# Kernel optimization log

Measured on AMD Instinct MI355X. Metric: run time of the kernel, lower is better.

The kernel has to match this reference:

```python
import jax, jax.numpy as jnp
import numpy as np

BN_EPS = 1e-5


def setup_inputs() -> dict:
    key = jax.random.key(0)
    ks = jax.random.split(key, 8)
    B, N, D = 16, 16384, 64
    NP, NS = 1024, 32
    inp = {
        "xyz": jax.random.normal(ks[0], (B, 3, N), dtype=jnp.float32),
        "points": jax.random.normal(ks[1], (B, D, N), dtype=jnp.float32),
        "fps_init": jax.random.randint(ks[2], (B,), 0, N, dtype=jnp.int32),
        "group_idx": jax.random.randint(ks[3], (B, NP, NS), 0, N, dtype=jnp.int32),
    }
    chans = [67, 64, 128, 128]
    for i in range(3):
        cin, cout = chans[i], chans[i + 1]
        wk = jax.random.fold_in(ks[4], i)
        inp[f"W{i}"] = jax.random.normal(wk, (cout, cin), dtype=jnp.float32) * (1.0 / np.sqrt(cin))
        inp[f"b{i}"] = jnp.zeros((cout,), dtype=jnp.float32)
        inp[f"g{i}"] = jnp.ones((cout,), dtype=jnp.float32)
        inp[f"be{i}"] = jnp.zeros((cout,), dtype=jnp.float32)
    return inp


def _fps(x, init_far, npoint):
    # x: [B,N,3]; iterative furthest point sampling, npoint sequential steps
    B, N, _ = x.shape

    def step(carry, _):
        dist, far = carry
        c = jnp.take_along_axis(x, far[:, None, None], axis=1)  # [B,1,3]
        d = jnp.sum((x - c) ** 2, axis=-1)                       # [B,N]
        dist = jnp.minimum(dist, d)
        return (dist, jnp.argmax(dist, axis=-1).astype(far.dtype)), far

    init = (jnp.full((B, N), 1e10, dtype=x.dtype), init_far)
    _, cents = jax.lax.scan(step, init, None, length=npoint)
    return cents.T  # [B, npoint]


def _conv_bn_relu(h, W, b, g, be):
    # h: [B, np, ns, Cin]; 1x1 conv == channel matmul; BN (training stats) over (B,np,ns)
    y = jnp.einsum('bskc,oc->bsko', h, W) + b
    m = y.mean(axis=(0, 1, 2))
    v = y.var(axis=(0, 1, 2))
    y = (y - m) * jax.lax.rsqrt(v + BN_EPS) * g + be
    return jax.nn.relu(y)


def reference(xyz, points, fps_init, group_idx,
              W0, b0, g0, be0, W1, b1, g1, be1, W2, b2, g2, be2):
    x = jnp.transpose(xyz, (0, 2, 1))     # [B,N,3]
    p = jnp.transpose(points, (0, 2, 1))  # [B,N,D]
    B, N, _ = x.shape
    NP, NS = group_idx.shape[1], group_idx.shape[2]

    cents = _fps(x, fps_init, NP)                                   # [B,NP]
    new_xyz = jnp.take_along_axis(x, cents[:, :, None], axis=1)     # [B,NP,3]

    flat = group_idx.reshape(B, NP * NS)
    gx = jnp.take_along_axis(x, flat[:, :, None], axis=1).reshape(B, NP, NS, 3)
    gp = jnp.take_along_axis(p, flat[:, :, None], axis=1).reshape(B, NP, NS, -1)
    h = jnp.concatenate([gx, gp], axis=-1)  # [B,NP,NS,67]

    h = _conv_bn_relu(h, W0, b0, g0, be0)
    h = _conv_bn_relu(h, W1, b1, g1, be1)
    h = _conv_bn_relu(h, W2, b2, g2, be2)
    new_points = h.max(axis=2)              # max over nsample -> [B,NP,Cout]

    return jnp.transpose(new_xyz, (0, 2, 1)), jnp.transpose(new_points, (0, 2, 1))
```

## Files before the change

kernel.cpp:

```cpp
#include <hip/hip_runtime.h>

typedef short bf16x8 __attribute__((ext_vector_type(8)));
typedef float f32x4 __attribute__((ext_vector_type(4)));
typedef float f32x2 __attribute__((ext_vector_type(2)));
typedef unsigned short u16;
typedef unsigned int u32;
typedef unsigned long long u64;

#define NPTS 16384
#define NPOINT 1024
#define STOT 524288
#define NCB 240
#define NW  960

__device__ __forceinline__ u16 f2bf(float f){
  u32 u = __builtin_bit_cast(u32, f);
  u += 0x7fffu + ((u >> 16) & 1u);
  return (u16)(u >> 16);
}
__device__ __forceinline__ float bf2f(u16 u){
  u32 x = ((u32)u) << 16;
  return __builtin_bit_cast(float, x);
}

template<int CTRL>
__device__ __forceinline__ float dpp_maxf(float v){
  int x = __builtin_amdgcn_update_dpp(0, __builtin_bit_cast(int, v), CTRL, 0xf, 0xf, true);
  return fmaxf(v, __builtin_bit_cast(float, x));
}
template<int CTRL>
__device__ __forceinline__ u64 dpp_max(u64 key){
  u32 lo = (u32)key, hi = (u32)(key >> 32);
  u32 lo1 = (u32)__builtin_amdgcn_update_dpp(0, (int)lo, CTRL, 0xf, 0xf, true);
  u32 hi1 = (u32)__builtin_amdgcn_update_dpp(0, (int)hi, CTRL, 0xf, 0xf, true);
  u64 k1 = ((u64)hi1 << 32) | (u64)lo1;
  return (k1 > key) ? k1 : key;
}
__device__ __forceinline__ u64 packkey(float d, int idx){
  return ((u64)__builtin_bit_cast(u32, d) << 32) | (u64)(u32)(~(u32)idx);
}

__device__ __forceinline__ void arrive(u32* c){
  __hip_atomic_fetch_add(c, 1u, __ATOMIC_RELEASE, __HIP_MEMORY_SCOPE_AGENT);
}
__device__ __forceinline__ void waitc(u32* c, u32 tgt){
  while (__hip_atomic_load(c, __ATOMIC_ACQUIRE, __HIP_MEMORY_SCOPE_AGENT) < tgt)
    __builtin_amdgcn_s_sleep(16);
}

struct FpsS  { u32 rec[2][16][48]; uint2 kk[2][16]; float cbuf[NPOINT][3]; };
struct ConvS { float lsum[128]; float lsqr[128]; float av[128]; float dv[128]; };
union SMemU  { FpsS fps; ConvS conv; };

__device__ __forceinline__ bf16x8 load_bn_relu(const u16* __restrict__ row, int ko,
                                               const float* __restrict__ av,
                                               const float* __restrict__ dv){
  uint4 r = *(const uint4*)(row + ko);
  u32 w[4] = {r.x, r.y, r.z, r.w};
  bf16x8 out;
#pragma unroll
  for (int jj = 0; jj < 8; jj++){
    u16 us = (u16)(w[jj >> 1] >> ((jj & 1) * 16));
    float h = fmaxf(fmaf(av[ko + jj], bf2f(us), dv[ko + jj]), 0.f);
    out[jj] = (short)f2bf(h);
  }
  return out;
}

__global__ void zero_kernel(u32* __restrict__ ctrs){
  if (threadIdx.x < 64) ctrs[threadIdx.x] = 0;
}

__global__ __launch_bounds__(1024, 4) void mega_kernel(
    const float* __restrict__ xyz, const float* __restrict__ points,
    const int* __restrict__ finit, const int* __restrict__ gidx,
    const float* __restrict__ W0, const float* __restrict__ g0v, const float* __restrict__ be0,
    const float* __restrict__ W1, const float* __restrict__ g1v, const float* __restrict__ be1,
    const float* __restrict__ W2, const float* __restrict__ g2v, const float* __restrict__ be2,
    float* __restrict__ out0, float* __restrict__ out1,
    u16* __restrict__ XP, u16* __restrict__ y0, u16* __restrict__ y1,
    float* __restrict__ maxb, float* __restrict__ minb,
    float* __restrict__ statsF,
    u16* __restrict__ W0bf, u16* __restrict__ W1bf, u16* __restrict__ W2bf,
    u32* __restrict__ ctrs){
  __shared__ SMemU sm;
  const int t = threadIdx.x;
  const int wave = t >> 6, lane = t & 63;

  if (blockIdx.x < 16){
    const int b = blockIdx.x;
    const float* xb = xyz + (size_t)b * 3 * NPTS;
    f32x2 px[8], py[8], pz[8], dist[8];
#pragma unroll
    for (int j = 0; j < 8; j++){
      f32x2 x, y, z;
#pragma unroll
      for (int h = 0; h < 2; h++){
        int n = ((2*j + h) << 10) + t;
        x[h] = xb[n];
        y[h] = xb[NPTS + n];
        z[h] = xb[2*NPTS + n];
      }
      px[j] = x; py[j] = y; pz[j] = z;
      f32x2 big = {1e10f, 1e10f};
      dist[j] = big;
    }
    const int far0 = finit[b];
    float ccx = xb[far0], ccy = xb[NPTS + far0], ccz = xb[2*NPTS + far0];

    for (int it = 0; it < NPOINT; it++){
      const int p = it & 1;
      if (t == 0){
        sm.fps.cbuf[it][0] = ccx;
        sm.fps.cbuf[it][1] = ccy;
        sm.fps.cbuf[it][2] = ccz;
      }
      float bv = -1.f; int bk = 0;
      {
#pragma clang fp contract(off)
        f32x2 cx2 = {ccx, ccx}, cy2 = {ccy, ccy}, cz2 = {ccz, ccz};
#pragma unroll
        for (int j = 0; j < 8; j++){
          f32x2 dx = px[j] - cx2;
          f32x2 dy = py[j] - cy2;
          f32x2 dz = pz[j] - cz2;
          f32x2 dd = dx*dx + dy*dy + dz*dz;
          f32x2 dm = __builtin_elementwise_min(dist[j], dd);
          dist[j] = dm;
          bool g0 = dm.x > bv;
          bv = g0 ? dm.x : bv;  bk = g0 ? (2*j)   : bk;
          bool g1 = dm.y > bv;
          bv = g1 ? dm.y : bv;  bk = g1 ? (2*j+1) : bk;
        }
      }
      float m = bv;
      m = dpp_maxf<0xB1>(m);
      m = dpp_maxf<0x4E>(m);
      m = dpp_maxf<0x141>(m);
      m = dpp_maxf<0x140>(m);
      m = dpp_maxf<0x142>(m);
      m = dpp_maxf<0x143>(m);
      float ms = __builtin_bit_cast(float, __builtin_amdgcn_readlane(__builtin_bit_cast(int, m), 63));
      u64 mk = __ballot(bv == ms);
      int wl;
      if (__popcll(mk) == 1){
        wl = (int)__builtin_ctzll(mk);
      } else {
        u64 key = packkey(bv, (bk << 10) + t);
        key = dpp_max<0xB1>(key); key = dpp_max<0x4E>(key);
        key = dpp_max<0x141>(key); key = dpp_max<0x140>(key);
        key = dpp_max<0x142>(key); key = dpp_max<0x143>(key);
        u32 lo = (u32)__builtin_amdgcn_readlane((int)(u32)key, 63);
        wl = (int)((~lo) & 63u);
      }
      if (lane == wl){
        u32* r = &sm.fps.rec[p][wave][0];
#pragma unroll
        for (int j = 0; j < 8; j++){
          *(f32x2*)(r + 2*j)      = px[j];
          *(f32x2*)(r + 16 + 2*j) = py[j];
          *(f32x2*)(r + 32 + 2*j) = pz[j];
        }
        u64 key = packkey(bv, (bk << 10) + t);
        sm.fps.kk[p][wave] = make_uint2((u32)key, (u32)(key >> 32));
      }
      __syncthreads();
      uint2 wkk = sm.fps.kk[p][lane & 15];
      u64 gk = ((u64)wkk.y << 32) | (u64)wkk.x;
      gk = dpp_max<0xB1>(gk); gk = dpp_max<0x4E>(gk);
      gk = dpp_max<0x141>(gk); gk = dpp_max<0x140>(gk);
      u32 n = ~(u32)gk;
      int w    = (int)((n >> 6) & 15u);
      int kwin = (int)(n >> 10);
      const u32* rr = &sm.fps.rec[p][w][0];
      ccx = *(const float*)(rr + kwin);
      ccy = *(const float*)(rr + 16 + kwin);
      ccz = *(const float*)(rr + 32 + kwin);
    }
    for (int i = t; i < 3 * NPOINT; i += 1024){
      int cc = i >> 10, itt = i & 1023;
      out0[((size_t)b*3 + cc)*NPOINT + itt] = sm.fps.cbuf[itt][cc];
    }
    return;
  }

  const int cb = blockIdx.x - 16;
  const int lw = wave & 3, g = wave >> 2;
  const int Wk = cb*4 + g;
  const int lrow = lane & 15, lq = lane >> 4;
  float* bsum0 = statsF;          float* bsqr0 = statsF + 8192;
  float* bsum1 = statsF + 16384;  float* bsqr1 = statsF + 24576;
  float* bsum2 = statsF + 32768;  float* bsqr2 = statsF + 40960;
  float* a0 = statsF + 49152;       float* d0 = a0 + 128;
  float* a1 = statsF + 49152 + 256; float* d1 = a1 + 128;
  float* a2 = statsF + 49152 + 512; float* d2 = a2 + 128;

  for (u32 idx = (u32)cb*1024u + t; idx < 16u*16384u; idx += (u32)NCB*1024u){
    u32 b = idx >> 14, n = idx & 16383u;
    const float* xb = xyz + (size_t)b*3*NPTS + n;
    const float* pb = points + (size_t)b*64*NPTS + n;
    u16* dst = XP + ((size_t)b*NPTS + n)*96;
#pragma unroll
    for (int half = 0; half < 2; half++){
      u32 w[24];
#pragma unroll
      for (int q = 0; q < 24; q++){
        int c0 = half*48 + 2*q, c1 = c0 + 1;
        float f0 = (c0 < 3) ? xb[(size_t)c0*NPTS] : (c0 < 67) ? pb[(size_t)(c0-3)*NPTS] : 0.f;
        float f1 = (c1 < 3) ? xb[(size_t)c1*NPTS] : (c1 < 67) ? pb[(size_t)(c1-3)*NPTS] : 0.f;
        w[q] = (u32)f2bf(f0) | ((u32)f2bf(f1) << 16);
      }
#pragma unroll
      for (int q = 0; q < 6; q++){
        uint4 v; v.x = w[4*q]; v.y = w[4*q+1]; v.z = w[4*q+2]; v.w = w[4*q+3];
        *(uint4*)(dst + half*48 + q*8) = v;
      }
    }
  }
  if (cb == 0){
    for (int i = t; i < 64*96; i += 1024){
      int nn = i / 96, kk = i % 96;
      W0bf[i] = (kk < 67) ? f2bf(W0[nn*67 + kk]) : (u16)0;
    }
    for (int i = t; i < 128*64; i += 1024) W1bf[i] = f2bf(W1[i]);
    for (int i = t; i < 128*128; i += 1024) W2bf[i] = f2bf(W2[i]);
  }
  if (cb == 1){
    for (int i = t; i < 49152; i += 1024) statsF[i] = 0.f;
  }
  __threadfence();
  __syncthreads();
  if (t == 0){ arrive(&ctrs[0]); waitc(&ctrs[0], NCB); }
  __syncthreads();

  if (t < 128){ sm.conv.lsum[t] = 0.f; sm.conv.lsqr[t] = 0.f; }
  __syncthreads();
  for (int j2 = Wk; j2 < 4096; j2 += NW){
    const int b = j2 >> 8;
    const size_t srow = (size_t)j2 * 128;
    const int gbase = b*32768 + (j2 & 255)*128;
    const int m0 = lw*32 + lrow, m1 = m0 + 16;
    const int p0 = gidx[gbase + m0];
    const int p1 = gidx[gbase + m1];
    const bf16x8* ar0 = (const bf16x8*)(XP + ((size_t)b*NPTS + p0)*96);
    const bf16x8* ar1 = (const bf16x8*)(XP + ((size_t)b*NPTS + p1)*96);
    f32x4 acc[2][4];
#pragma unroll
    for (int mt = 0; mt < 2; mt++)
#pragma unroll
      for (int nt = 0; nt < 4; nt++){ f32x4 z = {0.f,0.f,0.f,0.f}; acc[mt][nt] = z; }
#pragma unroll
    for (int ks = 0; ks < 3; ks++){
      bf16x8 af0 = ar0[ks*4 + lq];
      bf16x8 af1 = ar1[ks*4 + lq];
#pragma unroll
      for (int nt = 0; nt < 4; nt++){
        bf16x8 bb = *(const bf16x8*)(W0bf + (nt*16 + lrow)*96 + ks*32 + lq*8);
        acc[0][nt] = __builtin_amdgcn_mfma_f32_16x16x32_bf16(af0, bb, acc[0][nt], 0, 0, 0);
        acc[1][nt] = __builtin_amdgcn_mfma_f32_16x16x32_bf16(af1, bb, acc[1][nt], 0, 0, 0);
      }
    }
#pragma unroll
    for (int nt = 0; nt < 4; nt++){
      float s = 0.f, s2 = 0.f;
#pragma unroll
      for (int mt = 0; mt < 2; mt++){
#pragma unroll
        for (int i = 0; i < 4; i++){
          float u = acc[mt][nt][i];
          s += u; s2 = fmaf(u, u, s2);
          int m = lw*32 + mt*16 + lq*4 + i;
          y0[(srow + m)*64 + nt*16 + lrow] = f2bf(u);
        }
      }
      s  += __shfl_xor(s, 16, 64);  s  += __shfl_xor(s, 32, 64);
      s2 += __shfl_xor(s2, 16, 64); s2 += __shfl_xor(s2, 32, 64);
      if (lane < 16){ atomicAdd(&sm.conv.lsum[nt*16 + lane], s); atomicAdd(&sm.conv.lsqr[nt*16 + lane], s2); }
    }
  }
  __syncthreads();
  if (t < 64){
    atomicAdd(&bsum0[(cb & 63)*128 + t], sm.conv.lsum[t]);
    atomicAdd(&bsqr0[(cb & 63)*128 + t], sm.conv.lsqr[t]);
  }
  __threadfence();
  __syncthreads();
  if (t == 0) arrive(&ctrs[1]);
  if (cb == 0){
    if (t == 0) waitc(&ctrs[1], NCB);
    __syncthreads();
    if (t < 64){
      float s = 0.f, s2 = 0.f;
      for (int k = 0; k < 64; k++){ s += bsum0[k*128 + t]; s2 += bsqr0[k*128 + t]; }
      const float inv = 1.f / (float)STOT;
      float m = s * inv, v = s2 * inv - m*m;
      float aa = g0v[t] / sqrtf(v + 1e-5f);
      a0[t] = aa; d0[t] = be0[t] - m*aa;
    }
    __threadfence();
    __syncthreads();
    if (t == 0) arrive(&ctrs[2]);
  }
  if (t == 0) waitc(&ctrs[2], 1);
  __syncthreads();

  if (t < 128){ sm.conv.lsum[t] = 0.f; sm.conv.lsqr[t] = 0.f; }
  if (t < 64){ sm.conv.av[t] = a0[t]; sm.conv.dv[t] = d0[t]; }
  __syncthreads();
  for (int j2 = Wk; j2 < 4096; j2 += NW){
    const size_t srow = (size_t)j2 * 128;
    const int m0 = lw*32 + lrow, m1 = m0 + 16;
    const u16* row0 = y0 + (srow + m0)*64;
    const u16* row1 = y0 + (srow + m1)*64;
    f32x4 acc[2][8];
#pragma unroll
    for (int mt = 0; mt < 2; mt++)
#pragma unroll
      for (int nt = 0; nt < 8; nt++){ f32x4 z = {0.f,0.f,0.f,0.f}; acc[mt][nt] = z; }
#pragma unroll
    for (int ks = 0; ks < 2; ks++){
      const int ko = ks*32 + lq*8;
      bf16x8 af0 = load_bn_relu(row0, ko, sm.conv.av, sm.conv.dv);
      bf16x8 af1 = load_bn_relu(row1, ko, sm.conv.av, sm.conv.dv);
#pragma unroll
      for (int nt = 0; nt < 8; nt++){
        bf16x8 bb = *(const bf16x8*)(W1bf + (nt*16 + lrow)*64 + ko);
        acc[0][nt] = __builtin_amdgcn_mfma_f32_16x16x32_bf16(af0, bb, acc[0][nt], 0, 0, 0);
        acc[1][nt] = __builtin_amdgcn_mfma_f32_16x16x32_bf16(af1, bb, acc[1][nt], 0, 0, 0);
      }
    }
#pragma unroll
    for (int nt = 0; nt < 8; nt++){
      float s = 0.f, s2 = 0.f;
#pragma unroll
      for (int mt = 0; mt < 2; mt++){
#pragma unroll
        for (int i = 0; i < 4; i++){
          float u = acc[mt][nt][i];
          s += u; s2 = fmaf(u, u, s2);
          int m = lw*32 + mt*16 + lq*4 + i;
          y1[(srow + m)*128 + nt*16 + lrow] = f2bf(u);
        }
      }
      s  += __shfl_xor(s, 16, 64);  s  += __shfl_xor(s, 32, 64);
      s2 += __shfl_xor(s2, 16, 64); s2 += __shfl_xor(s2, 32, 64);
      if (lane < 16){ atomicAdd(&sm.conv.lsum[nt*16 + lane], s); atomicAdd(&sm.conv.lsqr[nt*16 + lane], s2); }
    }
  }
  __syncthreads();
  if (t < 128){
    atomicAdd(&bsum1[(cb & 63)*128 + t], sm.conv.lsum[t]);
    atomicAdd(&bsqr1[(cb & 63)*128 + t], sm.conv.lsqr[t]);
  }
  __threadfence();
  __syncthreads();
  if (t == 0) arrive(&ctrs[3]);
  if (cb == 0){
    if (t == 0) waitc(&ctrs[3], NCB);
    __syncthreads();
    if (t < 128){
      float s = 0.f, s2 = 0.f;
      for (int k = 0; k < 64; k++){ s += bsum1[k*128 + t]; s2 += bsqr1[k*128 + t]; }
      const float inv = 1.f / (float)STOT;
      float m = s * inv, v = s2 * inv - m*m;
      float aa = g1v[t] / sqrtf(v + 1e-5f);
      a1[t] = aa; d1[t] = be1[t] - m*aa;
    }
    __threadfence();
    __syncthreads();
    if (t == 0) arrive(&ctrs[4]);
  }
  if (t == 0) waitc(&ctrs[4], 1);
  __syncthreads();

  if (t < 128){ sm.conv.lsum[t] = 0.f; sm.conv.lsqr[t] = 0.f;
                sm.conv.av[t] = a1[t]; sm.conv.dv[t] = d1[t]; }
  __syncthreads();
  for (int j2 = Wk; j2 < 4096; j2 += NW){
    const size_t srow = (size_t)j2 * 128;
    const int m0 = lw*32 + lrow, m1 = m0 + 16;
    const u16* row0 = y1 + (srow + m0)*128;
    const u16* row1 = y1 + (srow + m1)*128;
    f32x4 acc[2][8];
#pragma unroll
    for (int mt = 0; mt < 2; mt++)
#pragma unroll
      for (int nt = 0; nt < 8; nt++){ f32x4 z = {0.f,0.f,0.f,0.f}; acc[mt][nt] = z; }
#pragma unroll
    for (int ks = 0; ks < 4; ks++){
      const int ko = ks*32 + lq*8;
      bf16x8 af0 = load_bn_relu(row0, ko, sm.conv.av, sm.conv.dv);
      bf16x8 af1 = load_bn_relu(row1, ko, sm.conv.av, sm.conv.dv);
#pragma unroll
      for (int nt = 0; nt < 8; nt++){
        bf16x8 bb = *(const bf16x8*)(W2bf + (nt*16 + lrow)*128 + ko);
        acc[0][nt] = __builtin_amdgcn_mfma_f32_16x16x32_bf16(af0, bb, acc[0][nt], 0, 0, 0);
        acc[1][nt] = __builtin_amdgcn_mfma_f32_16x16x32_bf16(af1, bb, acc[1][nt], 0, 0, 0);
      }
    }
#pragma unroll
    for (int nt = 0; nt < 8; nt++){
      float s = 0.f, s2 = 0.f, mx = -3.4e38f, mn = 3.4e38f;
#pragma unroll
      for (int mt = 0; mt < 2; mt++){
#pragma unroll
        for (int i = 0; i < 4; i++){
          float u = acc[mt][nt][i];
          s += u; s2 = fmaf(u, u, s2);
          mx = fmaxf(mx, u); mn = fminf(mn, u);
        }
      }
      s  += __shfl_xor(s, 16, 64);  s  += __shfl_xor(s, 32, 64);
      s2 += __shfl_xor(s2, 16, 64); s2 += __shfl_xor(s2, 32, 64);
      mx = fmaxf(mx, __shfl_xor(mx, 16, 64)); mx = fmaxf(mx, __shfl_xor(mx, 32, 64));
      mn = fminf(mn, __shfl_xor(mn, 16, 64)); mn = fminf(mn, __shfl_xor(mn, 32, 64));
      if (lane < 16){
        size_t gi = ((size_t)j2*4 + lw)*128 + nt*16 + lane;
        maxb[gi] = mx; minb[gi] = mn;
        atomicAdd(&sm.conv.lsum[nt*16 + lane], s); atomicAdd(&sm.conv.lsqr[nt*16 + lane], s2);
      }
    }
  }
  __syncthreads();
  if (t < 128){
    atomicAdd(&bsum2[(cb & 63)*128 + t], sm.conv.lsum[t]);
    atomicAdd(&bsqr2[(cb & 63)*128 + t], sm.conv.lsqr[t]);
  }
  __threadfence();
  __syncthreads();
  if (t == 0) arrive(&ctrs[5]);
  if (cb == 0){
    if (t == 0) waitc(&ctrs[5], NCB);
    __syncthreads();
    if (t < 128){
      float s = 0.f, s2 = 0.f;
      for (int k = 0; k < 64; k++){ s += bsum2[k*128 + t]; s2 += bsqr2[k*128 + t]; }
      const float inv = 1.f / (float)STOT;
      float m = s * inv, v = s2 * inv - m*m;
      float aa = g2v[t] / sqrtf(v + 1e-5f);
      a2[t] = aa; d2[t] = be2[t] - m*aa;
    }
    __threadfence();
    __syncthreads();
    if (t == 0) arrive(&ctrs[6]);
  }
  if (t == 0) waitc(&ctrs[6], 1);
  __syncthreads();

  for (u32 e = (u32)cb*1024u + t; e < 16u*1024u*128u; e += (u32)NCB*1024u){
    u32 np = e & 1023u;
    u32 c  = (e >> 10) & 127u;
    u32 b  = e >> 17;
    size_t gi = ((size_t)b*1024 + np)*128 + c;
    float a = a2[c];
    float v = (a >= 0.f) ? maxb[gi] : minb[gi];
    out1[((size_t)b*128 + c)*1024 + np] = fmaxf(fmaf(a, v, d2[c]), 0.f);
  }
}

extern "C" void kernel_launch(void* const* d_in, const int* in_sizes, int n_in,
                              void* d_out, int out_size, void* d_ws, size_t ws_size,
                              hipStream_t stream) {
  const float* xyz    = (const float*)d_in[0];
  const float* points = (const float*)d_in[1];
  const int*   finit  = (const int*)d_in[2];
  const int*   gidx   = (const int*)d_in[3];
  const float* W0  = (const float*)d_in[4];
  const float* g0v = (const float*)d_in[6];
  const float* be0 = (const float*)d_in[7];
  const float* W1  = (const float*)d_in[8];
  const float* g1v = (const float*)d_in[10];
  const float* be1 = (const float*)d_in[11];
  const float* W2  = (const float*)d_in[12];
  const float* g2v = (const float*)d_in[14];
  const float* be2 = (const float*)d_in[15];

  float* out0 = (float*)d_out;
  float* out1 = out0 + 16*3*NPOINT;

  char* ws = (char*)d_ws;
  u16* y1 = (u16*)ws;
  u16* XP = (u16*)ws;
  u16* y0 = (u16*)(ws + 134217728);
  float* maxb = (float*)(ws + 134217728);
  float* minb = (float*)(ws + 134217728 + 8388608);
  float* statsF = (float*)(ws + 201326592);
  u16* W0bf = (u16*)(ws + 201326592 + 49920*4);
  u16* W1bf = W0bf + 64*96;
  u16* W2bf = W1bf + 128*64;
  u32* ctrs = (u32*)(ws + 205782016);

  zero_kernel<<<1, 64, 0, stream>>>(ctrs);
  mega_kernel<<<256, 1024, 0, stream>>>(
      xyz, points, finit, gidx,
      W0, g0v, be0, W1, g1v, be1, W2, g2v, be2,
      out0, out1, XP, y0, y1, maxb, minb, statsF,
      W0bf, W1bf, W2bf, ctrs);
}
```

Baseline: 1.972 ms.

## Restructure FPS to 512 threads with y/z coordinates in LDS and readlane broadcast

```diff
diff --git a/kernel.cpp b/kernel.cpp
--- a/kernel.cpp
+++ b/kernel.cpp
@@ -2,7 +2,6 @@
 
 typedef short bf16x8 __attribute__((ext_vector_type(8)));
 typedef float f32x4 __attribute__((ext_vector_type(4)));
-typedef float f32x2 __attribute__((ext_vector_type(2)));
 typedef unsigned short u16;
 typedef unsigned int u32;
 typedef unsigned long long u64;
@@ -12,6 +11,9 @@
 #define STOT 524288
 #define NCB 240
 #define NW  960
+#define FTHREADS 512
+#define FWAVES 8
+#define KPT 32
 
 __device__ __forceinline__ u16 f2bf(float f){
   u32 u = __builtin_bit_cast(u32, f);
@@ -48,7 +50,13 @@
     __builtin_amdgcn_s_sleep(16);
 }
 
-struct FpsS  { u32 rec[2][16][48]; uint2 kk[2][16]; float cbuf[NPOINT][3]; };
+struct FpsS  {
+  float ylds[KPT][FTHREADS];
+  float zlds[KPT][FTHREADS];
+  float cbuf[NPOINT][3];
+  float kxA[2][FWAVES], kyA[2][FWAVES], kzA[2][FWAVES];
+  uint2 kkA[2][FWAVES];
+};
 struct ConvS { float lsum[128]; float lsqr[128]; float av[128]; float dv[128]; };
 union SMemU  { FpsS fps; ConvS conv; };
 
@@ -88,25 +96,21 @@
   const int wave = t >> 6, lane = t & 63;
 
   if (blockIdx.x < 16){
+    if (t >= FTHREADS) return;
     const int b = blockIdx.x;
     const float* xb = xyz + (size_t)b * 3 * NPTS;
-    f32x2 px[8], py[8], pz[8], dist[8];
-#pragma unroll
-    for (int j = 0; j < 8; j++){
-      f32x2 x, y, z;
-#pragma unroll
-      for (int h = 0; h < 2; h++){
-        int n = ((2*j + h) << 10) + t;
-        x[h] = xb[n];
-        y[h] = xb[NPTS + n];
-        z[h] = xb[2*NPTS + n];
-      }
-      px[j] = x; py[j] = y; pz[j] = z;
-      f32x2 big = {1e10f, 1e10f};
-      dist[j] = big;
+    float px[KPT], dist[KPT];
+#pragma unroll
+    for (int k = 0; k < KPT; k++){
+      int n = (k << 9) + t;
+      px[k] = xb[n];
+      sm.fps.ylds[k][t] = xb[NPTS + n];
+      sm.fps.zlds[k][t] = xb[2*NPTS + n];
+      dist[k] = 1e10f;
     }
     const int far0 = finit[b];
     float ccx = xb[far0], ccy = xb[NPTS + far0], ccz = xb[2*NPTS + far0];
+    __syncthreads();
 
     for (int it = 0; it < NPOINT; it++){
       const int p = it & 1;
@@ -118,19 +122,16 @@
       float bv = -1.f; int bk = 0;
       {
 #pragma clang fp contract(off)
-        f32x2 cx2 = {ccx, ccx}, cy2 = {ccy, ccy}, cz2 = {ccz, ccz};
-#pragma unroll
-        for (int j = 0; j < 8; j++){
-          f32x2 dx = px[j] - cx2;
-          f32x2 dy = py[j] - cy2;
-          f32x2 dz = pz[j] - cz2;
-          f32x2 dd = dx*dx + dy*dy + dz*dz;
-          f32x2 dm = __builtin_elementwise_min(dist[j], dd);
-          dist[j] = dm;
-          bool g0 = dm.x > bv;
-          bv = g0 ? dm.x : bv;  bk = g0 ? (2*j)   : bk;
-          bool g1 = dm.y > bv;
-          bv = g1 ? dm.y : bv;  bk = g1 ? (2*j+1) : bk;
+#pragma unroll
+        for (int k = 0; k < KPT; k++){
+          float dx = px[k] - ccx;
+          float dy = sm.fps.ylds[k][t] - ccy;
+          float dz = sm.fps.zlds[k][t] - ccz;
+          float dd = dx*dx + dy*dy + dz*dz;
+          float dm = fminf(dist[k], dd);
+          dist[k] = dm;
+          bool g = dm > bv;
+          bv = g ? dm : bv;  bk = g ? k : bk;
         }
       }
       float m = bv;
@@ -146,7 +147,7 @@
       if (__popcll(mk) == 1){
         wl = (int)__builtin_ctzll(mk);
       } else {
-        u64 key = packkey(bv, (bk << 10) + t);
+        u64 key = packkey(bv, (bk << 9) + t);
         key = dpp_max<0xB1>(key); key = dpp_max<0x4E>(key);
         key = dpp_max<0x141>(key); key = dpp_max<0x140>(key);
         key = dpp_max<0x142>(key); key = dpp_max<0x143>(key);
@@ -154,30 +155,31 @@
         wl = (int)((~lo) & 63u);
       }
       if (lane == wl){
-        u32* r = &sm.fps.rec[p][wave][0];
-#pragma unroll
-        for (int j = 0; j < 8; j++){
-          *(f32x2*)(r + 2*j)      = px[j];
-          *(f32x2*)(r + 16 + 2*j) = py[j];
-          *(f32x2*)(r + 32 + 2*j) = pz[j];
-        }
-        u64 key = packkey(bv, (bk << 10) + t);
-        sm.fps.kk[p][wave] = make_uint2((u32)key, (u32)(key >> 32));
+        int kk2 = bk;
+        float sx = px[0];
+#pragma unroll
+        for (int k2 = 1; k2 < KPT; k2++){ bool e = (kk2 == k2); sx = e ? px[k2] : sx; }
+        sm.fps.kxA[p][wave] = sx;
+        sm.fps.kyA[p][wave] = sm.fps.ylds[kk2][t];
+        sm.fps.kzA[p][wave] = sm.fps.zlds[kk2][t];
+        u64 key = packkey(bv, (bk << 9) + t);
+        sm.fps.kkA[p][wave] = make_uint2((u32)key, (u32)(key >> 32));
       }
       __syncthreads();
-      uint2 wkk = sm.fps.kk[p][lane & 15];
+      const int sl = lane & 7;
+      uint2 wkk = sm.fps.kkA[p][sl];
+      u32 fx = __builtin_bit_cast(u32, sm.fps.kxA[p][sl]);
+      u32 fy = __builtin_bit_cast(u32, sm.fps.kyA[p][sl]);
+      u32 fz = __builtin_bit_cast(u32, sm.fps.kzA[p][sl]);
       u64 gk = ((u64)wkk.y << 32) | (u64)wkk.x;
-      gk = dpp_max<0xB1>(gk); gk = dpp_max<0x4E>(gk);
-      gk = dpp_max<0x141>(gk); gk = dpp_max<0x140>(gk);
-      u32 n = ~(u32)gk;
-      int w    = (int)((n >> 6) & 15u);
-      int kwin = (int)(n >> 10);
-      const u32* rr = &sm.fps.rec[p][w][0];
-      ccx = *(const float*)(rr + kwin);
-      ccy = *(const float*)(rr + 16 + kwin);
-      ccz = *(const float*)(rr + 32 + kwin);
-    }
-    for (int i = t; i < 3 * NPOINT; i += 1024){
+      gk = dpp_max<0xB1>(gk); gk = dpp_max<0x4E>(gk); gk = dpp_max<0x141>(gk);
+      u32 n = (u32)__builtin_amdgcn_readfirstlane((int)(~(u32)gk));
+      int w = (int)((n >> 6) & 7u);
+      ccx = __builtin_bit_cast(float, __builtin_amdgcn_readlane((int)fx, w));
+      ccy = __builtin_bit_cast(float, __builtin_amdgcn_readlane((int)fy, w));
+      ccz = __builtin_bit_cast(float, __builtin_amdgcn_readlane((int)fz, w));
+    }
+    for (int i = t; i < 3 * NPOINT; i += FTHREADS){
       int cc = i >> 10, itt = i & 1023;
       out0[((size_t)b*3 + cc)*NPOINT + itt] = sm.fps.cbuf[itt][cc];
     }
```

New measurement: 2.309 ms. 17.1% more time.

## Replace per-iteration FPS block barrier with LDS sequence-tag spin handoff

Applied to the files above, without the earlier changes.

```diff
diff --git a/kernel.cpp b/kernel.cpp
--- a/kernel.cpp
+++ b/kernel.cpp
@@ -48,7 +48,12 @@
     __builtin_amdgcn_s_sleep(16);
 }
 
-struct FpsS  { u32 rec[2][16][48]; uint2 kk[2][16]; float cbuf[NPOINT][3]; };
+struct FpsS  {
+  float cbuf[NPOINT][3];
+  float kx[8][16], ky[8][16], kz[8][16];
+  u32 klo[8][16], khi[8][16];
+  u32 wseq[8][16];
+};
 struct ConvS { float lsum[128]; float lsqr[128]; float av[128]; float dv[128]; };
 union SMemU  { FpsS fps; ConvS conv; };
 
@@ -105,11 +110,13 @@
       f32x2 big = {1e10f, 1e10f};
       dist[j] = big;
     }
+    if (t < 128) sm.fps.wseq[t >> 4][t & 15] = 0xFFFFFFFFu;
     const int far0 = finit[b];
     float ccx = xb[far0], ccy = xb[NPTS + far0], ccz = xb[2*NPTS + far0];
+    __syncthreads();
 
     for (int it = 0; it < NPOINT; it++){
-      const int p = it & 1;
+      const int s = it & 7;
       if (t == 0){
         sm.fps.cbuf[it][0] = ccx;
         sm.fps.cbuf[it][1] = ccy;
@@ -154,28 +161,44 @@
         wl = (int)((~lo) & 63u);
       }
       if (lane == wl){
-        u32* r = &sm.fps.rec[p][wave][0];
-#pragma unroll
-        for (int j = 0; j < 8; j++){
-          *(f32x2*)(r + 2*j)      = px[j];
-          *(f32x2*)(r + 16 + 2*j) = py[j];
-          *(f32x2*)(r + 32 + 2*j) = pz[j];
+        int kk2 = bk;
+        float sx = px[0].x, sy = py[0].x, sz = pz[0].x;
+#pragma unroll
+        for (int k = 1; k < 16; k++){
+          bool e = (kk2 == k);
+          float vx = px[k>>1][k&1], vy = py[k>>1][k&1], vz = pz[k>>1][k&1];
+          sx = e ? vx : sx; sy = e ? vy : sy; sz = e ? vz : sz;
         }
         u64 key = packkey(bv, (bk << 10) + t);
-        sm.fps.kk[p][wave] = make_uint2((u32)key, (u32)(key >> 32));
-      }
-      __syncthreads();
-      uint2 wkk = sm.fps.kk[p][lane & 15];
-      u64 gk = ((u64)wkk.y << 32) | (u64)wkk.x;
-      gk = dpp_max<0xB1>(gk); gk = dpp_max<0x4E>(gk);
-      gk = dpp_max<0x141>(gk); gk = dpp_max<0x140>(gk);
-      u32 n = ~(u32)gk;
-      int w    = (int)((n >> 6) & 15u);
-      int kwin = (int)(n >> 10);
-      const u32* rr = &sm.fps.rec[p][w][0];
-      ccx = *(const float*)(rr + kwin);
-      ccy = *(const float*)(rr + 16 + kwin);
-      ccz = *(const float*)(rr + 32 + kwin);
+        sm.fps.kx[s][wave] = sx;
+        sm.fps.ky[s][wave] = sy;
+        sm.fps.kz[s][wave] = sz;
+        sm.fps.klo[s][wave] = (u32)key;
+        sm.fps.khi[s][wave] = (u32)(key >> 32);
+        __hip_atomic_store(&sm.fps.wseq[s][wave], (u32)it,
+                           __ATOMIC_RELEASE, __HIP_MEMORY_SCOPE_WORKGROUP);
+      }
+      if (it < NPOINT - 1){
+        const int sl = lane & 15;
+        u32 tag;
+        do {
+          tag = __hip_atomic_load(&sm.fps.wseq[s][sl],
+                                  __ATOMIC_ACQUIRE, __HIP_MEMORY_SCOPE_WORKGROUP);
+        } while (!__all(tag == (u32)it));
+        u32 lo = sm.fps.klo[s][sl], hi = sm.fps.khi[s][sl];
+        u32 fx = __builtin_bit_cast(u32, sm.fps.kx[s][sl]);
+        u32 fy = __builtin_bit_cast(u32, sm.fps.ky[s][sl]);
+        u32 fz = __builtin_bit_cast(u32, sm.fps.kz[s][sl]);
+        u64 gk = ((u64)hi << 32) | (u64)lo;
+        gk = dpp_max<0xB1>(gk); gk = dpp_max<0x4E>(gk);
+        gk = dpp_max<0x141>(gk); gk = dpp_max<0x140>(gk);
+        u32 n = (u32)__builtin_amdgcn_readfirstlane((int)(~(u32)gk));
+        int w = (int)((n >> 6) & 15u);
+        ccx = __builtin_bit_cast(float, __builtin_amdgcn_readlane((int)fx, w));
+        ccy = __builtin_bit_cast(float, __builtin_amdgcn_readlane((int)fy, w));
+        ccz = __builtin_bit_cast(float, __builtin_amdgcn_readlane((int)fz, w));
+      }
+      if ((it & 7) == 7) __syncthreads();
     }
     for (int i = t; i < 3 * NPOINT; i += 1024){
       int cc = i >> 10, itt = i & 1023;
```

After: 2.397 ms. 21.6% more time.
